# Optimization experiments

Measured on AMD Instinct MI355X. Metric: run time of the kernel, lower is better.

## Reference

```python
import jax, jax.numpy as jnp
import numpy as np

B, T, C, HS = 8, 2048, 2048, 128  # batch, seq, n_embedding, head_size
THETA = 10000.0


def _rope_tables(dim, seq_len, theta=THETA):
    freqs = 1.0 / theta ** (jnp.arange(0, dim, 2, dtype=jnp.float32) / dim)  # [dim/2]
    t = jnp.arange(seq_len, dtype=jnp.float32)
    ang = jnp.outer(t, freqs)  # [T, dim/2]
    return jnp.cos(ang), jnp.sin(ang)


def _apply_rope(v, cos, sin):
    # v: [B,T,D]; pairs along last dim treated as complex (real=even, imag=odd)
    b, t, d = v.shape
    vr = v.reshape(b, t, d // 2, 2)
    x0, x1 = vr[..., 0], vr[..., 1]
    o0 = x0 * cos - x1 * sin
    o1 = x0 * sin + x1 * cos
    return jnp.stack([o0, o1], axis=-1).reshape(b, t, d)


def setup_inputs() -> dict:
    key = jax.random.key(0)
    k1, k2, k3, k4 = jax.random.split(key, 4)
    scale = 1.0 / np.sqrt(C)
    x = jax.random.normal(k1, (B, T, C), dtype=jnp.float32)
    Wk = jax.random.normal(k2, (C, HS), dtype=jnp.float32) * scale
    Wq = jax.random.normal(k3, (C, HS), dtype=jnp.float32) * scale
    Wv = jax.random.normal(k4, (C, HS), dtype=jnp.float32) * scale
    return {"x": x, "Wk": Wk, "Wq": Wq, "Wv": Wv}


def reference(x, Wk, Wq, Wv):
    b, t, _ = x.shape
    cos, sin = _rope_tables(HS, t)
    k = x @ Wk  # [B,T,HS]
    q = x @ Wq
    # Source: xq,xk = apply_rotary_emb(key, query); query,key = xq,xk
    # => scores = rope(q_proj) @ rope(k_proj)^T (standard causal attention)
    qr = _apply_rope(q, cos, sin)
    kr = _apply_rope(k, cos, sin)
    scores = jnp.einsum('btd,bsd->bts', qr, kr) * (HS ** -0.5)  # [B,T,T]
    causal = jnp.tril(jnp.ones((t, t), dtype=bool))
    scores = jnp.where(causal, scores, -jnp.inf)
    wei = jax.nn.softmax(scores, axis=-1)
    v = x @ Wv
    return jnp.einsum('bts,bsd->btd', wei, v)
```

## Files before the change

### kernel.cpp

```cpp
#include <hip/hip_runtime.h>

#define NB 8
#define NT 2048
#define NC 2048
#define NH 128

typedef short s8v __attribute__((ext_vector_type(8)));
typedef float f4  __attribute__((ext_vector_type(4)));

static __device__ __forceinline__ unsigned short f2bf(float f) {
    union { float f; unsigned int u; } v; v.f = f;
    unsigned int x = v.u;
    return (unsigned short)((x + 0x7FFFu + ((x >> 16) & 1u)) >> 16);
}

static __device__ __forceinline__ void gl2lds16(const void* g, void* lds_base) {
    __builtin_amdgcn_global_load_lds(
        (const __attribute__((address_space(1))) unsigned int*)g,
        (__attribute__((address_space(3))) unsigned int*)lds_base, 16, 0, 0);
}

__global__ __launch_bounds__(256) void wtrans_k(
    const float* __restrict__ Wk, const float* __restrict__ Wq,
    const float* __restrict__ Wv, unsigned short* __restrict__ wt)
{
    __shared__ float Ls[64][129];
    const int mat = blockIdx.y;
    const float* W = (mat == 0) ? Wq : (mat == 1) ? Wk : Wv;
    const int k0 = blockIdx.x * 64;
    const int t  = threadIdx.x;

    #pragma unroll
    for (int j = 0; j < 8; ++j) {
        int flat = j * 1024 + t * 4;
        int k = flat >> 7, n = flat & 127;
        f4 v = *reinterpret_cast<const f4*>(W + (size_t)(k0 + k) * NH + n);
        Ls[k][n] = v[0]; Ls[k][n + 1] = v[1]; Ls[k][n + 2] = v[2]; Ls[k][n + 3] = v[3];
    }
    __syncthreads();

    const int n = t >> 1, half = t & 1;
    unsigned short tmp[32];
    #pragma unroll
    for (int kk = 0; kk < 32; ++kk) tmp[kk] = f2bf(Ls[half * 32 + kk][n]);
    unsigned short* dst = wt + (size_t)mat * 262144 + (size_t)n * 2048 + k0 + half * 32;
    #pragma unroll
    for (int v = 0; v < 4; ++v)
        *reinterpret_cast<s8v*>(dst + v * 8) = *reinterpret_cast<s8v*>(tmp + v * 8);
}

__global__ __launch_bounds__(256) void proj_rope(
    const float* __restrict__ x, const unsigned short* __restrict__ wt,
    unsigned short* __restrict__ qws, unsigned short* __restrict__ kws,
    unsigned short* __restrict__ vtws)
{
    __shared__ char LDS[32768];
    char* XsB = LDS;
    char* BsB = LDS + 16384;

    const int mat  = blockIdx.y;
    const int wave = threadIdx.x >> 6;
    const int lane = threadIdx.x & 63;
    const int quad = lane >> 4, l16 = lane & 15;
    const int wm = wave >> 1, wn = wave & 1;
    const int M0 = blockIdx.x * 64;
    const unsigned short* wtm = wt + mat * (NH * NC);

    const float* xbase[4]; const unsigned short* bbase[4];
    const int bc = (lane & 7) ^ (lane >> 3);
    #pragma unroll
    for (int s = 0; s < 4; ++s) {
        const int xrow = wave * 16 + s * 4 + (lane >> 4);
        const int xcol = ((lane & 15) ^ (xrow & 15)) * 4;
        xbase[s] = x + (size_t)(M0 + xrow) * NC + xcol;
        const int brow = wave * 32 + s * 8 + (lane >> 3);
        bbase[s] = wtm + (size_t)brow * NC + bc * 8;
    }

    f4 acc[2][4];
    #pragma unroll
    for (int mi = 0; mi < 2; ++mi)
        #pragma unroll
        for (int ni = 0; ni < 4; ++ni)
            acc[mi][ni] = (f4){0.f, 0.f, 0.f, 0.f};

    for (int kk = 0; kk < NC; kk += 64) {
        #pragma unroll
        for (int s = 0; s < 4; ++s)
            gl2lds16(xbase[s] + kk, XsB + (wave * 4 + s) * 1024);
        #pragma unroll
        for (int s = 0; s < 4; ++s)
            gl2lds16(bbase[s] + kk, BsB + (wave * 4 + s) * 1024);
        __syncthreads();

        #pragma unroll
        for (int ksub = 0; ksub < 2; ++ksub) {
            s8v a[2];
            #pragma unroll
            for (int mi = 0; mi < 2; ++mi) {
                const int rb = (wm * 32 + mi * 16 + l16) * 256;
                const int p0 = (ksub * 8 + quad * 2) ^ l16;
                union { f4 f; unsigned int u[4]; } L, H;
                L.f = *reinterpret_cast<const f4*>(XsB + rb + p0 * 16);
                H.f = *reinterpret_cast<const f4*>(XsB + rb + (p0 ^ 1) * 16);
                union { s8v s; unsigned int u[4]; } A;
                A.u[0] = __builtin_amdgcn_perm(L.u[1], L.u[0], 0x07060302u);
                A.u[1] = __builtin_amdgcn_perm(L.u[3], L.u[2], 0x07060302u);
                A.u[2] = __builtin_amdgcn_perm(H.u[1], H.u[0], 0x07060302u);
                A.u[3] = __builtin_amdgcn_perm(H.u[3], H.u[2], 0x07060302u);
                a[mi] = A.s;
            }
            #pragma unroll
            for (int ni = 0; ni < 4; ++ni) {
                const int row2 = wn * 64 + ni * 16 + l16;
                const int pb = (ksub * 4 + quad) ^ (l16 & 7);
                s8v b = *reinterpret_cast<const s8v*>(BsB + row2 * 128 + pb * 16);
                acc[0][ni] = __builtin_amdgcn_mfma_f32_16x16x32_bf16(a[0], b, acc[0][ni], 0, 0, 0);
                acc[1][ni] = __builtin_amdgcn_mfma_f32_16x16x32_bf16(a[1], b, acc[1][ni], 0, 0, 0);
            }
        }
        __syncthreads();
    }

    const float cfreq = -0.10381025296f;
    #pragma unroll
    for (int mi = 0; mi < 2; ++mi) {
        #pragma unroll
        for (int ni = 0; ni < 4; ++ni) {
            const int col = wn * 64 + ni * 16 + l16;
            #pragma unroll
            for (int r = 0; r < 4; ++r) {
                const int row = M0 + wm * 32 + mi * 16 + quad * 4 + r;
                const int t   = row & (NT - 1);
                float v = acc[mi][ni][r];
                if (mat < 2) {
                    float other = __shfl_xor(v, 1, 64);
                    float freq  = exp2f(cfreq * (float)(col & ~1));
                    float ang   = (float)t * freq;
                    float sn = sinf(ang), cs = cosf(ang);
                    v = (col & 1) ? (other * sn + v * cs)
                                  : (v * cs - other * sn);
                }
                unsigned short bv = f2bf(v);
                if (mat == 0)      qws[(size_t)row * NH + col] = bv;
                else if (mat == 1) kws[(size_t)row * NH + col] = bv;
                else {
                    int b = row >> 11;
                    vtws[(size_t)b * (NH * NT) + (size_t)col * NT + t] = bv;
                }
            }
        }
    }
}

__global__ __launch_bounds__(256, 2) void attn_k(
    const unsigned short* __restrict__ qws, const unsigned short* __restrict__ kws,
    const unsigned short* __restrict__ vtws, float* __restrict__ out)
{
    __shared__ unsigned short P[4][32 * 64];
    __shared__ float Os[4][32][64];
    __shared__ float Ms[4][32], Ls[4][32], Lt[32];

    const int wave = threadIdx.x >> 6;
    const int lane = threadIdx.x & 63;
    const int quad = lane >> 4, l16 = lane & 15;
    const int b     = blockIdx.y;
    const int qrow0 = blockIdx.x * 32;
    const unsigned short* Q  = qws  + (size_t)b * NT * NH;
    const unsigned short* K  = kws  + (size_t)b * NT * NH;
    const unsigned short* Vt = vtws + (size_t)b * NH * NT;

    s8v qf[2][4];
    #pragma unroll
    for (int mi = 0; mi < 2; ++mi)
        #pragma unroll
        for (int ks = 0; ks < 4; ++ks)
            qf[mi][ks] = *reinterpret_cast<const s8v*>(
                Q + (size_t)(qrow0 + mi * 16 + l16) * NH + ks * 32 + quad * 8);

    float m[2][4], ls[2][4];
    f4 o[2][8];
    #pragma unroll
    for (int mi = 0; mi < 2; ++mi) {
        #pragma unroll
        for (int r = 0; r < 4; ++r) { m[mi][r] = -INFINITY; ls[mi][r] = 0.f; }
        #pragma unroll
        for (int dt = 0; dt < 8; ++dt) o[mi][dt] = (f4){0.f, 0.f, 0.f, 0.f};
    }

    const int nkt = (qrow0 >> 6) + 1;
    const float scale = 0.0883883476f;

    for (int kt = wave; kt < nkt; kt += 4) {
        const int kbase = kt * 64;
        const bool domask = (kt == nkt - 1);

        f4 s[2][4];
        #pragma unroll
        for (int nt = 0; nt < 4; ++nt) {
            f4 a0 = (f4){0.f, 0.f, 0.f, 0.f}, a1 = a0;
            #pragma unroll
            for (int ks = 0; ks < 4; ++ks) {
                s8v kf = *reinterpret_cast<const s8v*>(
                    K + (size_t)(kbase + nt * 16 + l16) * NH + ks * 32 + quad * 8);
                a0 = __builtin_amdgcn_mfma_f32_16x16x32_bf16(qf[0][ks], kf, a0, 0, 0, 0);
                a1 = __builtin_amdgcn_mfma_f32_16x16x32_bf16(qf[1][ks], kf, a1, 0, 0, 0);
            }
            s[0][nt] = a0; s[1][nt] = a1;
        }

        #pragma unroll
        for (int mi = 0; mi < 2; ++mi) {
            #pragma unroll
            for (int r = 0; r < 4; ++r) {
                const int trow = qrow0 + mi * 16 + quad * 4 + r;
                #pragma unroll
                for (int nt = 0; nt < 4; ++nt) {
                    float sv = s[mi][nt][r] * scale;
                    if (domask && (kbase + nt * 16 + l16 > trow)) sv = -INFINITY;
                    s[mi][nt][r] = sv;
                }
                float tm = fmaxf(fmaxf(s[mi][0][r], s[mi][1][r]),
                                 fmaxf(s[mi][2][r], s[mi][3][r]));
                #pragma unroll
                for (int off = 1; off < 16; off <<= 1)
                    tm = fmaxf(tm, __shfl_xor(tm, off, 64));
                const float mn = fmaxf(m[mi][r], tm);
                const float alpha = __expf(m[mi][r] - mn);
                m[mi][r] = mn;
                float rs = 0.f;
                #pragma unroll
                for (int nt = 0; nt < 4; ++nt) {
                    float p = __expf(s[mi][nt][r] - mn);
                    s[mi][nt][r] = p;
                    rs += p;
                }
                ls[mi][r] = ls[mi][r] * alpha + rs;
                #pragma unroll
                for (int dt = 0; dt < 8; ++dt) o[mi][dt][r] *= alpha;
            }
        }

        #pragma unroll
        for (int mi = 0; mi < 2; ++mi)
            #pragma unroll
            for (int nt = 0; nt < 4; ++nt)
                #pragma unroll
                for (int r = 0; r < 4; ++r) {
                    const int prow = mi * 16 + quad * 4 + r;
                    const int swz  = ((nt * 2 + (l16 >> 3)) ^ (prow & 7)) * 8 + (l16 & 7);
                    P[wave][prow * 64 + swz] = f2bf(s[mi][nt][r]);
                }

        #pragma unroll
        for (int ks2 = 0; ks2 < 2; ++ks2) {
            s8v pa[2];
            #pragma unroll
            for (int mi = 0; mi < 2; ++mi) {
                const int prow = mi * 16 + l16;
                const int pp = ((ks2 * 4 + quad) ^ (l16 & 7));
                pa[mi] = *reinterpret_cast<const s8v*>(&P[wave][prow * 64 + pp * 8]);
            }
            #pragma unroll
            for (int dt = 0; dt < 8; ++dt) {
                s8v vf = *reinterpret_cast<const s8v*>(
                    Vt + (size_t)(dt * 16 + l16) * NT + kbase + ks2 * 32 + quad * 8);
                o[0][dt] = __builtin_amdgcn_mfma_f32_16x16x32_bf16(pa[0], vf, o[0][dt], 0, 0, 0);
                o[1][dt] = __builtin_amdgcn_mfma_f32_16x16x32_bf16(pa[1], vf, o[1][dt], 0, 0, 0);
            }
        }
    }

    #pragma unroll
    for (int mi = 0; mi < 2; ++mi)
        #pragma unroll
        for (int r = 0; r < 4; ++r) {
            float v = ls[mi][r];
            #pragma unroll
            for (int off = 1; off < 16; off <<= 1) v += __shfl_xor(v, off, 64);
            ls[mi][r] = v;
        }

    if (l16 == 0) {
        #pragma unroll
        for (int mi = 0; mi < 2; ++mi)
            #pragma unroll
            for (int r = 0; r < 4; ++r) {
                Ms[wave][mi * 16 + quad * 4 + r] = m[mi][r];
                Ls[wave][mi * 16 + quad * 4 + r] = ls[mi][r];
            }
    }
    __syncthreads();

    #pragma unroll
    for (int mi = 0; mi < 2; ++mi)
        #pragma unroll
        for (int r = 0; r < 4; ++r) {
            const int row = mi * 16 + quad * 4 + r;
            float M = fmaxf(fmaxf(Ms[0][row], Ms[1][row]), fmaxf(Ms[2][row], Ms[3][row]));
            float sc = __expf(m[mi][r] - M);
            float lt = Ls[0][row] * __expf(Ms[0][row] - M) + Ls[1][row] * __expf(Ms[1][row] - M)
                     + Ls[2][row] * __expf(Ms[2][row] - M) + Ls[3][row] * __expf(Ms[3][row] - M);
            if (wave == 0 && l16 == 0) Lt[row] = lt;
            #pragma unroll
            for (int dt = 0; dt < 8; ++dt) o[mi][dt][r] *= sc;
        }

    const int rrow = threadIdx.x >> 3;
    const int cx   = (threadIdx.x & 7) * 8;
    #pragma unroll
    for (int h = 0; h < 2; ++h) {
        __syncthreads();
        #pragma unroll
        for (int mi = 0; mi < 2; ++mi)
            #pragma unroll
            for (int dtl = 0; dtl < 4; ++dtl)
                #pragma unroll
                for (int r = 0; r < 4; ++r)
                    Os[wave][mi * 16 + quad * 4 + r][dtl * 16 + l16] = o[mi][h * 4 + dtl][r];
        __syncthreads();
        f4 s0 = (f4){0.f, 0.f, 0.f, 0.f}, s1 = s0;
        #pragma unroll
        for (int w = 0; w < 4; ++w) {
            s0 += *reinterpret_cast<const f4*>(&Os[w][rrow][cx]);
            s1 += *reinterpret_cast<const f4*>(&Os[w][rrow][cx + 4]);
        }
        const float rl = 1.0f / Lt[rrow];
        float* dst = &out[((size_t)b * NT + qrow0 + rrow) * NH + h * 64 + cx];
        *reinterpret_cast<f4*>(dst)     = s0 * rl;
        *reinterpret_cast<f4*>(dst + 4) = s1 * rl;
    }
}

extern "C" void kernel_launch(void* const* d_in, const int* in_sizes, int n_in,
                              void* d_out, int out_size, void* d_ws, size_t ws_size,
                              hipStream_t stream) {
    const float* x  = (const float*)d_in[0];
    const float* Wk = (const float*)d_in[1];
    const float* Wq = (const float*)d_in[2];
    const float* Wv = (const float*)d_in[3];
    unsigned short* ws   = (unsigned short*)d_ws;
    unsigned short* wt   = ws;
    unsigned short* qws  = ws  + 786432;
    unsigned short* kws  = qws + 2097152;
    unsigned short* vtws = kws + 2097152;
    float* outp = (float*)d_out;

    wtrans_k<<<dim3(32, 3), 256, 0, stream>>>(Wk, Wq, Wv, wt);
    proj_rope<<<dim3(256, 3), 256, 0, stream>>>(x, wt, qws, kws, vtws);
    attn_k<<<dim3(64, 8), 256, 0, stream>>>(qws, kws, vtws, outp);
}
```

Baseline: 302.6 us.

## Convert x to bf16 during load and double the projection K-tile

The projection GEMM now reads x through registers and converts it to bf16 before the LDS store, so the A tile in LDS is half the size. The K-step per iteration grows from 64 to 128, halving the number of barrier rounds. The MFMA loop then reads bf16 A fragments directly instead of doing fp32 LDS reads plus perm per fragment. In exchange, the x loads are synchronous global loads that go through VGPRs rather than direct global-to-LDS loads, and LDS use rises to 48KB, which may reduce occupancy.

```diff
diff --git a/kernel.cpp b/kernel.cpp
--- a/kernel.cpp
+++ b/kernel.cpp
@@ -54,27 +54,39 @@
     unsigned short* __restrict__ qws, unsigned short* __restrict__ kws,
     unsigned short* __restrict__ vtws)
 {
-    __shared__ char LDS[32768];
-    char* XsB = LDS;
+    __shared__ char LDS[49152];
+    char* AsB = LDS;
     char* BsB = LDS + 16384;
 
     const int mat  = blockIdx.y;
-    const int wave = threadIdx.x >> 6;
-    const int lane = threadIdx.x & 63;
+    const int tid  = threadIdx.x;
+    const int wave = tid >> 6;
+    const int lane = tid & 63;
     const int quad = lane >> 4, l16 = lane & 15;
     const int wm = wave >> 1, wn = wave & 1;
     const int M0 = blockIdx.x * 64;
     const unsigned short* wtm = wt + mat * (NH * NC);
 
-    const float* xbase[4]; const unsigned short* bbase[4];
-    const int bc = (lane & 7) ^ (lane >> 3);
-    #pragma unroll
-    for (int s = 0; s < 4; ++s) {
-        const int xrow = wave * 16 + s * 4 + (lane >> 4);
-        const int xcol = ((lane & 15) ^ (xrow & 15)) * 4;
-        xbase[s] = x + (size_t)(M0 + xrow) * NC + xcol;
-        const int brow = wave * 32 + s * 8 + (lane >> 3);
-        bbase[s] = wtm + (size_t)brow * NC + bc * 8;
+    const float* asrc[8];
+    unsigned int adst[8];
+    #pragma unroll
+    for (int s = 0; s < 8; ++s) {
+        const int f   = tid + s * 256;
+        const int row = f >> 5;
+        const int kc  = (f & 31) * 4;
+        asrc[s] = x + (size_t)(M0 + row) * NC + kc;
+        const int c   = kc >> 3;
+        const int pos = c ^ (row & 15);
+        adst[s] = row * 256 + pos * 16 + (kc & 4) * 2;
+    }
+
+    const unsigned short* bsrc[8];
+    #pragma unroll
+    for (int s = 0; s < 8; ++s) {
+        const int j   = wave * 8 + s;
+        const int row = j * 4 + (lane >> 4);
+        const int c   = (lane & 15) ^ (row & 15);
+        bsrc[s] = wtm + (size_t)row * NC + c * 8;
     }
 
     f4 acc[2][4];
@@ -84,37 +96,35 @@
         for (int ni = 0; ni < 4; ++ni)
             acc[mi][ni] = (f4){0.f, 0.f, 0.f, 0.f};
 
-    for (int kk = 0; kk < NC; kk += 64) {
-        #pragma unroll
-        for (int s = 0; s < 4; ++s)
-            gl2lds16(xbase[s] + kk, XsB + (wave * 4 + s) * 1024);
-        #pragma unroll
-        for (int s = 0; s < 4; ++s)
-            gl2lds16(bbase[s] + kk, BsB + (wave * 4 + s) * 1024);
+    for (int kk = 0; kk < NC; kk += 128) {
+        #pragma unroll
+        for (int s = 0; s < 8; ++s)
+            gl2lds16(bsrc[s] + kk, BsB + (wave * 8 + s) * 1024);
+
+        #pragma unroll
+        for (int s = 0; s < 8; ++s) {
+            union { f4 f; unsigned int u[4]; } v;
+            v.f = *reinterpret_cast<const f4*>(asrc[s] + kk);
+            unsigned int d0 = __builtin_amdgcn_perm(v.u[1], v.u[0], 0x07060302u);
+            unsigned int d1 = __builtin_amdgcn_perm(v.u[3], v.u[2], 0x07060302u);
+            uint2 p; p.x = d0; p.y = d1;
+            *reinterpret_cast<uint2*>(AsB + adst[s]) = p;
+        }
         __syncthreads();
 
         #pragma unroll
-        for (int ksub = 0; ksub < 2; ++ksub) {
+        for (int ksub = 0; ksub < 4; ++ksub) {
+            const int c = ksub * 4 + quad;
             s8v a[2];
             #pragma unroll
             for (int mi = 0; mi < 2; ++mi) {
-                const int rb = (wm * 32 + mi * 16 + l16) * 256;
-                const int p0 = (ksub * 8 + quad * 2) ^ l16;
-                union { f4 f; unsigned int u[4]; } L, H;
-                L.f = *reinterpret_cast<const f4*>(XsB + rb + p0 * 16);
-                H.f = *reinterpret_cast<const f4*>(XsB + rb + (p0 ^ 1) * 16);
-                union { s8v s; unsigned int u[4]; } A;
-                A.u[0] = __builtin_amdgcn_perm(L.u[1], L.u[0], 0x07060302u);
-                A.u[1] = __builtin_amdgcn_perm(L.u[3], L.u[2], 0x07060302u);
-                A.u[2] = __builtin_amdgcn_perm(H.u[1], H.u[0], 0x07060302u);
-                A.u[3] = __builtin_amdgcn_perm(H.u[3], H.u[2], 0x07060302u);
-                a[mi] = A.s;
+                const int row = wm * 32 + mi * 16 + l16;
+                a[mi] = *reinterpret_cast<const s8v*>(AsB + row * 256 + (c ^ l16) * 16);
             }
             #pragma unroll
             for (int ni = 0; ni < 4; ++ni) {
                 const int row2 = wn * 64 + ni * 16 + l16;
-                const int pb = (ksub * 4 + quad) ^ (l16 & 7);
-                s8v b = *reinterpret_cast<const s8v*>(BsB + row2 * 128 + pb * 16);
+                s8v b = *reinterpret_cast<const s8v*>(BsB + row2 * 256 + (c ^ l16) * 16);
                 acc[0][ni] = __builtin_amdgcn_mfma_f32_16x16x32_bf16(a[0], b, acc[0][ni], 0, 0, 0);
                 acc[1][ni] = __builtin_amdgcn_mfma_f32_16x16x32_bf16(a[1], b, acc[1][ni], 0, 0, 0);
             }
```

Result: slower. 336.5 us (+11.2%).
